# Kernel optimization log

Hardware: AMD Instinct MI355X
Metric: run time of the kernel (lower is better)

Reference implementation:

```python
import jax, jax.numpy as jnp
import numpy as np

N_EDGE_TYPES = 25
EF = 2  # edge feature dim (excluding type)
HID = 10


def _edge_nn(et, ef, emb, wh, bh, wg, bg):
    # y = relu(emb[et] * (ef@Wh+bh) + (ef@Wg+bg)) -> [E, in*out]
    return jax.nn.relu(emb[et] * (ef @ wh + bh) + (ef @ wg + bg))


def _nnconv(x, et, ef, src, dst, emb, wh, bh, wg, bg, root, bias, in_c, out_c):
    n = x.shape[0]
    w = _edge_nn(et, ef, emb, wh, bh, wg, bg).reshape(-1, in_c, out_c)  # [E,in,out]
    msg = jnp.einsum('ei,eio->eo', x[src], w)                          # per-edge matmul
    s = jax.ops.segment_sum(msg, dst, num_segments=n)
    cnt = jax.ops.segment_sum(jnp.ones((src.shape[0],), x.dtype), dst, num_segments=n)
    agg = s / jnp.maximum(cnt, 1.0)[:, None]                           # scatter-mean
    return agg + x @ root + bias


def _make_params(key, in_c, out_c):
    ks = jax.random.split(key, 6)
    d = in_c * out_c
    s = 0.1
    return dict(
        emb=jax.random.normal(ks[0], (N_EDGE_TYPES, d), jnp.float32) * s,
        wh=jax.random.normal(ks[1], (EF, d), jnp.float32) * s,
        bh=jax.random.normal(ks[2], (d,), jnp.float32) * s,
        wg=jax.random.normal(ks[3], (EF, d), jnp.float32) * s,
        bg=jax.random.normal(ks[4], (d,), jnp.float32) * s,
        root=jax.random.normal(ks[5], (in_c, out_c), jnp.float32) * s,
        bias=jnp.zeros((out_c,), jnp.float32),
    )


def setup_inputs() -> dict:
    key = jax.random.key(0)
    ks = jax.random.split(key, 12)
    N, E, IN_C, OUT_C, B = 50000, 250000, 16, 16, 8
    inp = {
        'x': jax.random.normal(ks[0], (N, IN_C), jnp.float32),
        'edge_feat': jax.random.normal(ks[1], (E, EF), jnp.float32),
        'edge_type': jax.random.randint(ks[2], (E,), 0, N_EDGE_TYPES),
        'edge_src': jax.random.randint(ks[3], (E,), 0, N),
        'edge_dst': jax.random.randint(ks[4], (E,), 0, N),
        'cell_type': jax.random.randint(ks[5], (N,), 0, 3),
        'batch_ids': jnp.sort(jax.random.randint(ks[6], (N,), 0, B)),
        'batch_size': B,
    }
    for i, (ic, oc) in enumerate([(IN_C, HID), (HID, HID), (HID, OUT_C)], start=1):
        p = _make_params(ks[6 + i], ic, oc)
        for k, v in p.items():
            inp[f'{k}{i}'] = v
    return inp


def reference(x, edge_feat,
              emb1, wh1, bh1, wg1, bg1, root1, bias1,
              emb2, wh2, bh2, wg2, bg2, root2, bias2,
              emb3, wh3, bh3, wg3, bg3, root3, bias3,
              edge_type, edge_src, edge_dst, cell_type, batch_ids, batch_size):
    in_c, out_c = x.shape[1], root3.shape[1]
    h = _nnconv(x, edge_type, edge_feat, edge_src, edge_dst,
                emb1, wh1, bh1, wg1, bg1, root1, bias1, in_c, HID)
    h = jax.nn.relu(h)  # dropout is identity in eval mode
    h = _nnconv(h, edge_type, edge_feat, edge_src, edge_dst,
                emb2, wh2, bh2, wg2, bg2, root2, bias2, HID, HID)
    h = jax.nn.relu(h)
    h = _nnconv(h, edge_type, edge_feat, edge_src, edge_dst,
                emb3, wh3, bh3, wg3, bg3, root3, bias3, HID, out_c)
    h = jax.nn.relu(h)
    # scatter-mean pooling over nodes with cell_type==1, grouped by graph id
    gate = (cell_type == 1).astype(jnp.int32)
    idx = gate * (batch_ids.astype(jnp.int32) + 1)  # 0 = discarded bucket
    nseg = batch_size + 1
    s = jax.ops.segment_sum(h, idx, num_segments=nseg)
    cnt = jax.ops.segment_sum(jnp.ones((h.shape[0],), h.dtype), idx, num_segments=nseg)
    pooled = s / jnp.maximum(cnt, 1.0)[:, None]
    return pooled[1:batch_size + 1, :]  # [B, out_c]
```

## Files before the change

kernel.cpp:

```cpp
#include <hip/hip_runtime.h>

#define IN1 16
#define HIDC 10
#define OUT3 16
#define NTYPES 25
#define MAXB 32

__global__ __launch_bounds__(256) void zero2_kernel(int* __restrict__ a, int na,
                                                    int* __restrict__ b, int nb) {
  int i = blockIdx.x * blockDim.x + threadIdx.x;
  int s = gridDim.x * blockDim.x;
  for (int j = i; j < na; j += s) a[j] = 0;
  for (int j = i; j < nb; j += s) b[j] = 0;
}

__global__ __launch_bounds__(256) void hist_kernel(const int* __restrict__ edst,
                                                   int* __restrict__ deg,
                                                   int* __restrict__ pos, int E) {
  int e = blockIdx.x * blockDim.x + threadIdx.x;
  if (e < E) pos[e] = atomicAdd(&deg[edst[e]], 1);
}

__global__ __launch_bounds__(1024) void scan_kernel(const int4* __restrict__ deg4,
                                                    int* __restrict__ row_ptr, int N) {
  __shared__ int wsums[16];
  __shared__ int s_run;
  int tid = threadIdx.x, lane = tid & 63, wid = tid >> 6;
  if (tid == 0) s_run = 0;
  __syncthreads();
  int N4 = (N + 3) >> 2;
  for (int base = 0; base < N4; base += 1024) {
    int i4 = base + tid;
    int4 v = make_int4(0, 0, 0, 0);
    if (i4 < N4) v = deg4[i4];
    int idx0 = i4 * 4;
    if (idx0 + 1 >= N) v.y = 0;
    if (idx0 + 2 >= N) v.z = 0;
    if (idx0 + 3 >= N) v.w = 0;
    int s = v.x + v.y + v.z + v.w;
    int x = s;
    #pragma unroll
    for (int off = 1; off < 64; off <<= 1) {
      int y = __shfl_up(x, off);
      if (lane >= off) x += y;
    }
    if (lane == 63) wsums[wid] = x;
    __syncthreads();
    if (tid < 16) {
      int w = wsums[tid];
      #pragma unroll
      for (int off = 1; off < 16; off <<= 1) {
        int y = __shfl_up(w, off);
        if (tid >= off) w += y;
      }
      wsums[tid] = w;
    }
    __syncthreads();
    int excl = x - s + ((wid > 0) ? wsums[wid - 1] : 0) + s_run;
    int total = wsums[15];
    if (idx0 < N) row_ptr[idx0] = excl;
    if (idx0 + 1 < N) row_ptr[idx0 + 1] = excl + v.x;
    if (idx0 + 2 < N) row_ptr[idx0 + 2] = excl + v.x + v.y;
    if (idx0 + 3 < N) row_ptr[idx0 + 3] = excl + v.x + v.y + v.z;
    __syncthreads();
    if (tid == 0) s_run += total;
    __syncthreads();
  }
  if (threadIdx.x == 0) row_ptr[N] = s_run;
}

__global__ __launch_bounds__(256) void permute_kernel(
    const int* __restrict__ edst, const int* __restrict__ esrc,
    const int* __restrict__ et, const float2* __restrict__ ef,
    const int* __restrict__ row_ptr, const int* __restrict__ pos,
    int4* __restrict__ edges, int E) {
  int e = blockIdx.x * blockDim.x + threadIdx.x;
  if (e >= E) return;
  int d = edst[e];
  int idx = row_ptr[d] + pos[e];
  float2 f = ef[e];
  int4 r;
  r.x = esrc[e];
  r.y = et[e];
  r.z = __float_as_int(f.x);
  r.w = __float_as_int(f.y);
  edges[idx] = r;
}

template<int IN_C, int O, bool POOL, int BS>
__global__ __launch_bounds__(BS) void layer_kernel(
    const float* __restrict__ xin,
    const int4* __restrict__ edges,
    const int* __restrict__ row_ptr,
    const float* __restrict__ emb,
    const float* __restrict__ wh, const float* __restrict__ bh,
    const float* __restrict__ wg, const float* __restrict__ bg,
    const float* __restrict__ root,
    const float* __restrict__ bias,
    float* __restrict__ hout,
    const int* __restrict__ ctype, const int* __restrict__ bids,
    float* __restrict__ pcnt,
    int N, int B)
{
  constexpr int D = IN_C * O;
  constexpr int ESTR = D + 8;
  constexpr int NPB = BS / 16;
  __shared__ float4 s_pa[D];
  __shared__ float2 s_pb[D];
  __shared__ float s_emb[NTYPES * ESTR];
  __shared__ float s_root[D];
  __shared__ float s_bias[O];
  __shared__ float s_psum[POOL ? (MAXB * 16) : 1];
  __shared__ float s_pcnt[POOL ? MAXB : 1];

  int tid = threadIdx.x;
  for (int k = tid; k < D; k += BS) {
    s_pa[k] = make_float4(wh[k], wh[D + k], wg[k], wg[D + k]);
    s_pb[k] = make_float2(bh[k], bg[k]);
    s_root[k] = root[k];
  }
  for (int k = tid; k < NTYPES * D; k += BS) {
    int t = k / D, j = k - t * D;
    s_emb[t * ESTR + j] = emb[k];
  }
  if (tid < O) s_bias[tid] = bias[tid];
  if (POOL) {
    for (int i = tid; i < MAXB * 16; i += BS) s_psum[i] = 0.f;
    for (int i = tid; i < MAXB; i += BS) s_pcnt[i] = 0.f;
  }
  __syncthreads();

  int nl = tid >> 4;
  int o = tid & 15;
  int oc = (O == 16) ? o : ((o < O) ? o : 0);
  int n = blockIdx.x * NPB + nl;

  float acc = 0.f;
  int start = 0, end = 0;
  if (n < N) { start = row_ptr[n]; end = row_ptr[n + 1]; }
  for (int e = start; e < end; ++e) {
    int4 r = edges[e];
    int src = r.x, t = r.y;
    float f0 = __int_as_float(r.z), f1 = __int_as_float(r.w);
    const float* __restrict__ xr = xin + (size_t)src * IN_C;
    const float* __restrict__ er = s_emb + t * ESTR;
    #pragma unroll
    for (int i = 0; i < IN_C; ++i) {
      int k = i * O + oc;
      float4 a = s_pa[k];
      float2 b = s_pb[k];
      float h = fmaf(f0, a.x, fmaf(f1, a.y, b.x));
      float g = fmaf(f0, a.z, fmaf(f1, a.w, b.y));
      float w = fmaxf(fmaf(er[k], h, g), 0.f);
      acc = fmaf(xr[i], w, acc);
    }
  }

  if (n < N && o < O) {
    float inv = 1.0f / fmaxf((float)(end - start), 1.0f);
    float v = fmaf(acc, inv, s_bias[o]);
    const float* __restrict__ xr = xin + (size_t)n * IN_C;
    #pragma unroll
    for (int i = 0; i < IN_C; ++i) v = fmaf(xr[i], s_root[i * O + o], v);
    v = fmaxf(v, 0.f);
    if (!POOL) {
      hout[(size_t)n * O + o] = v;
    } else {
      if (ctype[n] == 1) {
        int b = bids[n];
        atomicAdd(&s_psum[b * 16 + o], v);
        if (o == 0) atomicAdd(&s_pcnt[b], 1.0f);
      }
    }
  }

  if (POOL) {
    __syncthreads();
    for (int i = tid; i < B * 16; i += BS) {
      float v = s_psum[i];
      if (v != 0.f) atomicAdd(&hout[i], v);
    }
    for (int i = tid; i < B; i += BS) {
      float c = s_pcnt[i];
      if (c != 0.f) atomicAdd(&pcnt[i], c);
    }
  }
}

__global__ __launch_bounds__(256) void finalize_kernel(
    const float* __restrict__ psum, const float* __restrict__ pcnt,
    float* __restrict__ out, int B) {
  int i = blockIdx.x * blockDim.x + threadIdx.x;
  if (i >= B * OUT3) return;
  int b = i / OUT3;
  out[i] = psum[i] / fmaxf(pcnt[b], 1.0f);
}

extern "C" void kernel_launch(void* const* d_in, const int* in_sizes, int n_in,
                              void* d_out, int out_size, void* d_ws, size_t ws_size,
                              hipStream_t stream)
{
  const float* x     = (const float*)d_in[0];
  const float* ef    = (const float*)d_in[1];
  const int*   et    = (const int*)d_in[2];
  const int*   esrc  = (const int*)d_in[3];
  const int*   edst  = (const int*)d_in[4];
  const int*   ctype = (const int*)d_in[5];
  const int*   bids  = (const int*)d_in[6];
  const float* emb1 = (const float*)d_in[8];
  const float* wh1  = (const float*)d_in[9];
  const float* bh1  = (const float*)d_in[10];
  const float* wg1  = (const float*)d_in[11];
  const float* bg1  = (const float*)d_in[12];
  const float* root1= (const float*)d_in[13];
  const float* bias1= (const float*)d_in[14];
  const float* emb2 = (const float*)d_in[15];
  const float* wh2  = (const float*)d_in[16];
  const float* bh2  = (const float*)d_in[17];
  const float* wg2  = (const float*)d_in[18];
  const float* bg2  = (const float*)d_in[19];
  const float* root2= (const float*)d_in[20];
  const float* bias2= (const float*)d_in[21];
  const float* emb3 = (const float*)d_in[22];
  const float* wh3  = (const float*)d_in[23];
  const float* bh3  = (const float*)d_in[24];
  const float* wg3  = (const float*)d_in[25];
  const float* bg3  = (const float*)d_in[26];
  const float* root3= (const float*)d_in[27];
  const float* bias3= (const float*)d_in[28];

  const int N = in_sizes[0] / IN1;
  const int E = in_sizes[2];
  const int B = out_size / OUT3;

  int4* edges   = (int4*)d_ws;
  int*  deg     = (int*)(edges + E);
  int*  pos     = deg + N;
  int*  row_ptr = pos + E;
  float* h1     = (float*)(row_ptr + (N + 1));
  float* h2     = h1 + (size_t)N * HIDC;
  float* psum   = h2 + (size_t)N * HIDC;
  float* pcnt   = psum + (size_t)B * 16;

  zero2_kernel<<<128, 256, 0, stream>>>(deg, N, (int*)psum, B * 16 + B);
  hist_kernel<<<(E + 255) / 256, 256, 0, stream>>>(edst, deg, pos, E);
  scan_kernel<<<1, 1024, 0, stream>>>((const int4*)deg, row_ptr, N);
  permute_kernel<<<(E + 255) / 256, 256, 0, stream>>>(
      edst, esrc, et, (const float2*)ef, row_ptr, pos, edges, E);

  const int g256 = (N + 15) / 16;
  layer_kernel<IN1, HIDC, false, 256><<<g256, 256, 0, stream>>>(
      x, edges, row_ptr, emb1, wh1, bh1, wg1, bg1, root1, bias1,
      h1, nullptr, nullptr, nullptr, N, B);
  layer_kernel<HIDC, HIDC, false, 256><<<g256, 256, 0, stream>>>(
      h1, edges, row_ptr, emb2, wh2, bh2, wg2, bg2, root2, bias2,
      h2, nullptr, nullptr, nullptr, N, B);

  const int g1024 = (N + 63) / 64;
  layer_kernel<HIDC, OUT3, true, 1024><<<g1024, 1024, 0, stream>>>(
      h2, edges, row_ptr, emb3, wh3, bh3, wg3, bg3, root3, bias3,
      psum, ctype, bids, pcnt, N, B);

  finalize_kernel<<<1, 256, 0, stream>>>(psum, pcnt, (float*)d_out, B);
}
```

Before: 281.1 us.

## Precombine edge-NN weights per type and split input channels across lanes

Adds a small pack kernel that folds emb, wh, wg, bh and bg into per-type coefficients A and C, so each edge weight becomes relu(f0*A0+f1*A1+C). This removes several FMAs and shared loads per weight element. The layer kernels now split input channels across 2 or 4 lane groups, combine the partial sums with shuffles, and use a grid-stride loop over a fixed 1024 blocks. Hidden activations are padded to a stride of 12 for vector loads, and the next edge record is prefetched. The trade-offs are larger shared-memory tables, an extra launch, and a dependence on the padding lanes of h1 and h2 being readable.

```diff
diff --git a/kernel.cpp b/kernel.cpp
--- a/kernel.cpp
+++ b/kernel.cpp
@@ -5,6 +5,7 @@
 #define OUT3 16
 #define NTYPES 25
 #define MAXB 32
+#define HSTR 12
 
 __global__ __launch_bounds__(256) void zero2_kernel(int* __restrict__ a, int na,
                                                     int* __restrict__ b, int nb) {
@@ -87,86 +88,139 @@
   edges[idx] = r;
 }
 
-template<int IN_C, int O, bool POOL, int BS>
-__global__ __launch_bounds__(BS) void layer_kernel(
+__global__ __launch_bounds__(256) void abc_pack_kernel(
+    const float* __restrict__ emb1, const float* __restrict__ wh1,
+    const float* __restrict__ bh1, const float* __restrict__ wg1, const float* __restrict__ bg1,
+    const float* __restrict__ emb2, const float* __restrict__ wh2,
+    const float* __restrict__ bh2, const float* __restrict__ wg2, const float* __restrict__ bg2,
+    const float* __restrict__ emb3, const float* __restrict__ wh3,
+    const float* __restrict__ bh3, const float* __restrict__ wg3, const float* __restrict__ bg3,
+    float2* __restrict__ gA1, float* __restrict__ gC1,
+    float2* __restrict__ gA2, float* __restrict__ gC2,
+    float2* __restrict__ gA3, float* __restrict__ gC3)
+{
+  int t = blockIdx.x;
+  for (int k = threadIdx.x; k < 160; k += 256) {
+    float e = emb1[t * 160 + k];
+    gA1[t * 160 + k] = make_float2(fmaf(e, wh1[k], wg1[k]), fmaf(e, wh1[160 + k], wg1[160 + k]));
+    gC1[t * 160 + k] = fmaf(e, bh1[k], bg1[k]);
+  }
+  for (int k = threadIdx.x; k < 120; k += 256) {
+    float a = 0.f, b = 0.f, c = 0.f;
+    if (k < 100) {
+      float e = emb2[t * 100 + k];
+      a = fmaf(e, wh2[k], wg2[k]);
+      b = fmaf(e, wh2[100 + k], wg2[100 + k]);
+      c = fmaf(e, bh2[k], bg2[k]);
+    }
+    gA2[t * 120 + k] = make_float2(a, b);
+    gC2[t * 120 + k] = c;
+  }
+  for (int k = threadIdx.x; k < 192; k += 256) {
+    float a = 0.f, b = 0.f, c = 0.f;
+    if (k < 160) {
+      float e = emb3[t * 160 + k];
+      a = fmaf(e, wh3[k], wg3[k]);
+      b = fmaf(e, wh3[160 + k], wg3[160 + k]);
+      c = fmaf(e, bh3[k], bg3[k]);
+    }
+    gA3[t * 192 + k] = make_float2(a, b);
+    gC3[t * 192 + k] = c;
+  }
+}
+
+template<int IN_C, int XSTR, int O, int IPG, int NPW, bool POOL>
+__global__ __launch_bounds__(256) void layer_kernel(
     const float* __restrict__ xin,
     const int4* __restrict__ edges,
     const int* __restrict__ row_ptr,
-    const float* __restrict__ emb,
-    const float* __restrict__ wh, const float* __restrict__ bh,
-    const float* __restrict__ wg, const float* __restrict__ bg,
+    const float2* __restrict__ gA2,
+    const float* __restrict__ gC,
     const float* __restrict__ root,
     const float* __restrict__ bias,
     float* __restrict__ hout,
     const int* __restrict__ ctype, const int* __restrict__ bids,
-    float* __restrict__ pcnt,
-    int N, int B)
+    float* __restrict__ pcnt, int N, int B)
 {
-  constexpr int D = IN_C * O;
-  constexpr int ESTR = D + 8;
-  constexpr int NPB = BS / 16;
-  __shared__ float4 s_pa[D];
-  __shared__ float2 s_pb[D];
-  __shared__ float s_emb[NTYPES * ESTR];
-  __shared__ float s_root[D];
+  constexpr int Dpad = XSTR * O;
+  constexpr int IC = XSTR / IPG;
+  __shared__ __align__(16) float2 s_A[NTYPES * Dpad];
+  __shared__ __align__(16) float s_C[NTYPES * Dpad];
+  __shared__ float s_root[IN_C * O];
   __shared__ float s_bias[O];
   __shared__ float s_psum[POOL ? (MAXB * 16) : 1];
   __shared__ float s_pcnt[POOL ? MAXB : 1];
 
   int tid = threadIdx.x;
-  for (int k = tid; k < D; k += BS) {
-    s_pa[k] = make_float4(wh[k], wh[D + k], wg[k], wg[D + k]);
-    s_pb[k] = make_float2(bh[k], bg[k]);
-    s_root[k] = root[k];
-  }
-  for (int k = tid; k < NTYPES * D; k += BS) {
-    int t = k / D, j = k - t * D;
-    s_emb[t * ESTR + j] = emb[k];
-  }
-  if (tid < O) s_bias[tid] = bias[tid];
-  if (POOL) {
-    for (int i = tid; i < MAXB * 16; i += BS) s_psum[i] = 0.f;
-    for (int i = tid; i < MAXB; i += BS) s_pcnt[i] = 0.f;
+  {
+    const float4* ga = (const float4*)gA2;
+    float4* sa = (float4*)s_A;
+    for (int k = tid; k < NTYPES * Dpad / 2; k += 256) sa[k] = ga[k];
+    const float4* gc = (const float4*)gC;
+    float4* sc = (float4*)s_C;
+    for (int k = tid; k < NTYPES * Dpad / 4; k += 256) sc[k] = gc[k];
+    for (int k = tid; k < IN_C * O; k += 256) s_root[k] = root[k];
+    if (tid < O) s_bias[tid] = bias[tid];
+    if (POOL) {
+      for (int i = tid; i < MAXB * 16; i += 256) s_psum[i] = 0.f;
+      for (int i = tid; i < MAXB; i += 256) s_pcnt[i] = 0.f;
+    }
   }
   __syncthreads();
 
-  int nl = tid >> 4;
-  int o = tid & 15;
-  int oc = (O == 16) ? o : ((o < O) ? o : 0);
-  int n = blockIdx.x * NPB + nl;
-
-  float acc = 0.f;
-  int start = 0, end = 0;
-  if (n < N) { start = row_ptr[n]; end = row_ptr[n + 1]; }
-  for (int e = start; e < end; ++e) {
-    int4 r = edges[e];
-    int src = r.x, t = r.y;
-    float f0 = __int_as_float(r.z), f1 = __int_as_float(r.w);
-    const float* __restrict__ xr = xin + (size_t)src * IN_C;
-    const float* __restrict__ er = s_emb + t * ESTR;
-    #pragma unroll
-    for (int i = 0; i < IN_C; ++i) {
-      int k = i * O + oc;
-      float4 a = s_pa[k];
-      float2 b = s_pb[k];
-      float h = fmaf(f0, a.x, fmaf(f1, a.y, b.x));
-      float g = fmaf(f0, a.z, fmaf(f1, a.w, b.y));
-      float w = fmaxf(fmaf(er[k], h, g), 0.f);
-      acc = fmaf(xr[i], w, acc);
-    }
-  }
-
-  if (n < N && o < O) {
-    float inv = 1.0f / fmaxf((float)(end - start), 1.0f);
-    float v = fmaf(acc, inv, s_bias[o]);
-    const float* __restrict__ xr = xin + (size_t)n * IN_C;
-    #pragma unroll
-    for (int i = 0; i < IN_C; ++i) v = fmaf(xr[i], s_root[i * O + o], v);
-    v = fmaxf(v, 0.f);
-    if (!POOL) {
-      hout[(size_t)n * O + o] = v;
-    } else {
-      if (ctype[n] == 1) {
+  int wave = tid >> 6, lane = tid & 63;
+  int slot = lane / (16 * IPG);
+  int rem = lane % (16 * IPG);
+  int ig = rem >> 4;
+  int o = rem & 15;
+  int oc = (o < O) ? o : (O - 1);
+  int kbase0 = (ig * IC) * O + oc;
+
+  int n0 = (blockIdx.x * 4 + wave) * NPW + slot;
+  int nstride = gridDim.x * 4 * NPW;
+  for (int n = n0; n < N; n += nstride) {
+    int start = row_ptr[n], end = row_ptr[n + 1];
+    float acc = 0.f;
+    int4 r = (start < end) ? edges[start] : make_int4(0, 0, 0, 0);
+    for (int e = start; e < end;) {
+      int4 cur = r;
+      ++e;
+      if (e < end) r = edges[e];
+      int src = cur.x, t = cur.y;
+      float f0 = __int_as_float(cur.z), f1 = __int_as_float(cur.w);
+      const float* __restrict__ xr = xin + (size_t)src * XSTR + ig * IC;
+      float xv[IC];
+      if (IC == 4) {
+        float4 v = *(const float4*)xr;
+        xv[0] = v.x; xv[1] = v.y; xv[2] = v.z; xv[3] = v.w;
+      } else {
+        const float2* x2 = (const float2*)xr;
+        float2 a = x2[0], b = x2[1], c = x2[2];
+        xv[0] = a.x; xv[1] = a.y; xv[2] = b.x; xv[3] = b.y; xv[4] = c.x; xv[5] = c.y;
+      }
+      int kb = t * Dpad + kbase0;
+      #pragma unroll
+      for (int j = 0; j < IC; ++j) {
+        int k = kb + j * O;
+        float2 ab = s_A[k];
+        float c = s_C[k];
+        float w = fmaxf(fmaf(f0, ab.x, fmaf(f1, ab.y, c)), 0.f);
+        acc = fmaf(xv[j], w, acc);
+      }
+    }
+    acc += __shfl_xor(acc, 16);
+    if (IPG == 4) acc += __shfl_xor(acc, 32);
+
+    if (ig == 0 && o < O) {
+      float inv = 1.0f / fmaxf((float)(end - start), 1.0f);
+      float v = fmaf(acc, inv, s_bias[o]);
+      const float* __restrict__ xr = xin + (size_t)n * XSTR;
+      #pragma unroll
+      for (int i = 0; i < IN_C; ++i) v = fmaf(xr[i], s_root[i * O + o], v);
+      v = fmaxf(v, 0.f);
+      if (!POOL) {
+        hout[(size_t)n * HSTR + o] = v;
+      } else if (ctype[n] == 1) {
         int b = bids[n];
         atomicAdd(&s_psum[b * 16 + o], v);
         if (o == 0) atomicAdd(&s_pcnt[b], 1.0f);
@@ -176,11 +230,11 @@
 
   if (POOL) {
     __syncthreads();
-    for (int i = tid; i < B * 16; i += BS) {
+    for (int i = tid; i < B * 16; i += 256) {
       float v = s_psum[i];
       if (v != 0.f) atomicAdd(&hout[i], v);
     }
-    for (int i = tid; i < B; i += BS) {
+    for (int i = tid; i < B; i += 256) {
       float c = s_pcnt[i];
       if (c != 0.f) atomicAdd(&pcnt[i], c);
     }
@@ -237,29 +291,34 @@
   int*  deg     = (int*)(edges + E);
   int*  pos     = deg + N;
   int*  row_ptr = pos + E;
-  float* h1     = (float*)(row_ptr + (N + 1));
-  float* h2     = h1 + (size_t)N * HIDC;
-  float* psum   = h2 + (size_t)N * HIDC;
+  int   np1r    = ((N + 1 + 3) / 4) * 4;
+  float* h1     = (float*)(row_ptr + np1r);
+  float* h2     = h1 + (size_t)N * HSTR;
+  float* psum   = h2 + (size_t)N * HSTR;
   float* pcnt   = psum + (size_t)B * 16;
+  float* pk     = pcnt + B;
+  float2* gA1 = (float2*)pk;
+  float*  gC1 = pk + 8000;
+  float2* gA2 = (float2*)(pk + 12000);
+  float*  gC2 = pk + 18000;
+  float2* gA3 = (float2*)(pk + 21000);
+  float*  gC3 = pk + 30600;
 
   zero2_kernel<<<128, 256, 0, stream>>>(deg, N, (int*)psum, B * 16 + B);
+  abc_pack_kernel<<<NTYPES, 256, 0, stream>>>(
+      emb1, wh1, bh1, wg1, bg1, emb2, wh2, bh2, wg2, bg2, emb3, wh3, bh3, wg3, bg3,
+      gA1, gC1, gA2, gC2, gA3, gC3);
   hist_kernel<<<(E + 255) / 256, 256, 0, stream>>>(edst, deg, pos, E);
   scan_kernel<<<1, 1024, 0, stream>>>((const int4*)deg, row_ptr, N);
   permute_kernel<<<(E + 255) / 256, 256, 0, stream>>>(
       edst, esrc, et, (const float2*)ef, row_ptr, pos, edges, E);
 
-  const int g256 = (N + 15) / 16;
-  layer_kernel<IN1, HIDC, false, 256><<<g256, 256, 0, stream>>>(
-      x, edges, row_ptr, emb1, wh1, bh1, wg1, bg1, root1, bias1,
-      h1, nullptr, nullptr, nullptr, N, B);
-  layer_kernel<HIDC, HIDC, false, 256><<<g256, 256, 0, stream>>>(
-      h1, edges, row_ptr, emb2, wh2, bh2, wg2, bg2, root2, bias2,
-      h2, nullptr, nullptr, nullptr, N, B);
-
-  const int g1024 = (N + 63) / 64;
-  layer_kernel<HIDC, OUT3, true, 1024><<<g1024, 1024, 0, stream>>>(
-      h2, edges, row_ptr, emb3, wh3, bh3, wg3, bg3, root3, bias3,
-      psum, ctype, bids, pcnt, N, B);
+  layer_kernel<IN1, 16, HIDC, 4, 1, false><<<1024, 256, 0, stream>>>(
+      x, edges, row_ptr, gA1, gC1, root1, bias1, h1, nullptr, nullptr, nullptr, N, B);
+  layer_kernel<HIDC, HSTR, HIDC, 2, 2, false><<<1024, 256, 0, stream>>>(
+      h1, edges, row_ptr, gA2, gC2, root2, bias2, h2, nullptr, nullptr, nullptr, N, B);
+  layer_kernel<HIDC, HSTR, OUT3, 2, 2, true><<<1024, 256, 0, stream>>>(
+      h2, edges, row_ptr, gA3, gC3, root3, bias3, psum, ctype, bids, pcnt, N, B);
 
   finalize_kernel<<<1, 256, 0, stream>>>(psum, pcnt, (float*)d_out, B);
 }
```

Measured after the change: 322.8 us. 1.15x slower.
